# Kernel optimization log

Hardware: AMD Instinct MI355X
Metric: run time of the kernel (lower is better)

Reference implementation:

```python
import jax, jax.numpy as jnp
import numpy as np


def setup_inputs() -> dict:
    key = jax.random.key(0)
    k1, k2 = jax.random.split(key)
    B, S, D = 4, 2048, 1024
    x = jax.random.normal(k1, (B, S, D), dtype=jnp.float32)
    # uniform initializer in keras is small; scale to keep softmax well-behaved
    kernel = jax.random.normal(k2, (3, D, D), dtype=jnp.float32) * 0.02
    return {"x": x, "kernel": kernel}


def reference(x, kernel):
    # x: [B, S, D], kernel: [3, D, D]
    D = x.shape[-1]
    q = jnp.einsum('bsd,de->bse', x, kernel[0])
    k = jnp.einsum('bsd,de->bse', x, kernel[1])
    v = jnp.einsum('bsd,de->bse', x, kernel[2])
    scores = jnp.einsum('bqe,bke->bqk', q, k) / jnp.sqrt(jnp.float32(D))
    attn = jax.nn.softmax(scores, axis=-1)
    return jnp.einsum('bqk,bke->bqe', attn, v)
```

## Files before the change

### kernel.cpp

```cpp
#include <hip/hip_runtime.h>
#include <hip/hip_bf16.h>
#include <cstdint>

typedef __bf16 bf16x8 __attribute__((ext_vector_type(8)));
typedef float f32x4 __attribute__((ext_vector_type(4)));

__device__ __forceinline__ unsigned short f2bf(float f) {
  union { float f; uint32_t u; } a; a.f = f;
  uint32_t r = a.u + 0x7fffu + ((a.u >> 16) & 1u);
  return (unsigned short)(r >> 16);
}
__device__ __forceinline__ uint32_t pk2(float lo, float hi) {
  return (uint32_t)f2bf(lo) | ((uint32_t)f2bf(hi) << 16);
}
__device__ __forceinline__ void gload_lds16(const unsigned short* g, unsigned short* l) {
  __builtin_amdgcn_global_load_lds(
      (const __attribute__((address_space(1))) void*)g,
      (__attribute__((address_space(3))) void*)l, 16, 0, 0);
}

__global__ void cast_all(const float* __restrict__ x, const float* __restrict__ W,
                         unsigned short* __restrict__ xb, unsigned short* __restrict__ Wt) {
  __shared__ float tileW[64][65];
  const int bx = blockIdx.x;
  const int t = threadIdx.x;
  if (bx < 4096) {
    size_t i = ((size_t)bx * 256 + t) * 8;
    float4 a = *(const float4*)(x + i);
    float4 b = *(const float4*)(x + i + 4);
    uint4 o;
    o.x = pk2(a.x, a.y);
    o.y = pk2(a.z, a.w);
    o.z = pk2(b.x, b.y);
    o.w = pk2(b.z, b.w);
    *(uint4*)(xb + i) = o;
  } else {
    const int b = bx - 4096;
    const int z = b >> 8;
    const int rest = b & 255;
    const int bxx = rest & 15, byy = rest >> 4;
    const float* Wz = W + (size_t)z * 1048576;
    unsigned short* Wtz = Wt + (size_t)z * 1048576;
    const int x0 = bxx * 64, y0 = byy * 64;
    {
      const int r = t >> 4;
      const int c = (t & 15) * 4;
#pragma unroll
      for (int p = 0; p < 64; p += 16) {
        float4 v = *(const float4*)(Wz + (size_t)(y0 + p + r) * 1024 + x0 + c);
        tileW[p + r][c + 0] = v.x;
        tileW[p + r][c + 1] = v.y;
        tileW[p + r][c + 2] = v.z;
        tileW[p + r][c + 3] = v.w;
      }
    }
    __syncthreads();
    {
      const int dc = (t & 7) * 8;
#pragma unroll
      for (int p = 0; p < 64; p += 32) {
        const int e = p + (t >> 3);
        uint4 o;
        o.x = pk2(tileW[dc + 0][e], tileW[dc + 1][e]);
        o.y = pk2(tileW[dc + 2][e], tileW[dc + 3][e]);
        o.z = pk2(tileW[dc + 4][e], tileW[dc + 5][e]);
        o.w = pk2(tileW[dc + 6][e], tileW[dc + 7][e]);
        *(uint4*)(Wtz + (size_t)(x0 + e) * 1024 + y0 + dc) = o;
      }
    }
  }
}

__global__ void __launch_bounds__(256)
gemm_qkv(const unsigned short* __restrict__ Aall,
         const unsigned short* __restrict__ Btall,
         unsigned short* __restrict__ QK, unsigned short* __restrict__ Vt,
         int K, int ldc, long sA, long sB, long sC) {
  __shared__ unsigned short As[2][4096];
  __shared__ unsigned short Bs[2][4096];
  const int t = threadIdx.x;
  const int lane = t & 63;
  const int quad = lane >> 4;
  const int l15 = lane & 15;
  const int wave = t >> 6;
  const int wm = (wave >> 1) * 64;
  const int wn = (wave & 1) * 64;
  const int z = blockIdx.z;

  const unsigned short* A = Aall + (size_t)z * sA + (size_t)blockIdx.x * 128 * K;
  const unsigned short* Bt = Btall + (size_t)z * sB + (size_t)blockIdx.y * 128 * K;

  const int srow = t >> 2;
  const int scol = (((t & 3) ^ ((srow >> 1) & 3)) * 8);
  const unsigned short* ga = A + (size_t)srow * K + scol;
  const unsigned short* gb = Bt + (size_t)srow * K + scol;
  const size_t rowskip = (size_t)64 * K;

  const int aOff = (wm + l15) * 32 + (quad ^ ((l15 >> 1) & 3)) * 8;
  const int bOff = (wn + l15) * 32 + (quad ^ ((l15 >> 1) & 3)) * 8;

  f32x4 acc[4][4];
#pragma unroll
  for (int i = 0; i < 4; i++)
#pragma unroll
    for (int j = 0; j < 4; j++) acc[i][j] = (f32x4){0.f, 0.f, 0.f, 0.f};

  gload_lds16(ga, &As[0][t * 8]);
  gload_lds16(ga + rowskip, &As[0][2048 + t * 8]);
  gload_lds16(gb, &Bs[0][t * 8]);
  gload_lds16(gb + rowskip, &Bs[0][2048 + t * 8]);

  int buf = 0;
  for (int k0 = 0; k0 < K; k0 += 32, buf ^= 1) {
    __syncthreads();
    if (k0 + 32 < K) {
      const int kn = k0 + 32;
      gload_lds16(ga + kn, &As[buf ^ 1][t * 8]);
      gload_lds16(ga + rowskip + kn, &As[buf ^ 1][2048 + t * 8]);
      gload_lds16(gb + kn, &Bs[buf ^ 1][t * 8]);
      gload_lds16(gb + rowskip + kn, &Bs[buf ^ 1][2048 + t * 8]);
    }
    const unsigned short* aB = &As[buf][aOff];
    const unsigned short* bB = &Bs[buf][bOff];
    bf16x8 a[4], b[4];
#pragma unroll
    for (int i = 0; i < 4; i++) a[i] = *(const bf16x8*)(aB + i * 512);
#pragma unroll
    for (int j = 0; j < 4; j++) b[j] = *(const bf16x8*)(bB + j * 512);
#pragma unroll
    for (int i = 0; i < 4; i++)
#pragma unroll
      for (int j = 0; j < 4; j++)
        acc[i][j] = __builtin_amdgcn_mfma_f32_16x16x32_bf16(a[i], b[j], acc[i][j], 0, 0, 0);
  }

  const int mbase = blockIdx.x * 128 + wm + quad * 4;
  const int nbase = blockIdx.y * 128 + wn + l15;

  if (z < 2) {
    unsigned short* C = QK + (size_t)z * sC;
#pragma unroll
    for (int mi = 0; mi < 4; mi++)
#pragma unroll
      for (int ni = 0; ni < 4; ni++) {
        const int m = mbase + mi * 16, n = nbase + ni * 16;
#pragma unroll
        for (int r = 0; r < 4; r++)
          C[(size_t)(m + r) * ldc + n] = f2bf(acc[mi][ni][r]);
      }
  } else {
#pragma unroll
    for (int mi = 0; mi < 4; mi++) {
      const int m = mbase + mi * 16;
      const int b = m >> 11, s = m & 2047;
#pragma unroll
      for (int ni = 0; ni < 4; ni++) {
        const int n = nbase + ni * 16;
        uint2 val;
        val.x = pk2(acc[mi][ni][0], acc[mi][ni][1]);
        val.y = pk2(acc[mi][ni][2], acc[mi][ni][3]);
        *(uint2*)(Vt + (size_t)b * 2097152 + (size_t)n * 2048 + s) = val;
      }
    }
  }
}

#define PHASE_OPEN() do { \
    __builtin_amdgcn_sched_barrier(0); \
    __builtin_amdgcn_s_barrier(); \
    asm volatile("s_waitcnt lgkmcnt(0)" ::: "memory"); \
    __builtin_amdgcn_sched_barrier(0); \
    __builtin_amdgcn_s_setprio(1); \
  } while (0)
#define PHASE_CLOSE() do { \
    __builtin_amdgcn_s_setprio(0); \
    __builtin_amdgcn_sched_barrier(0); \
    __builtin_amdgcn_s_barrier(); \
  } while (0)

__global__ void __launch_bounds__(512, 2)
gemm8_scores(const unsigned short* __restrict__ Aall,
             const unsigned short* __restrict__ Btall,
             unsigned short* __restrict__ Call, float* __restrict__ aux,
             int K, int ldc, long sA, long sB, long sC, float scale) {
  __shared__ unsigned short As[2][2][8192];
  __shared__ unsigned short Bs[2][2][8192];
  const int t = threadIdx.x;
  const int lane = t & 63;
  const int quad = lane >> 4;
  const int l15 = lane & 15;
  const int wave = t >> 6;
  const int wm = wave >> 2;
  const int wn = wave & 3;

  const int p_ = blockIdx.x + (blockIdx.y << 3) + (blockIdx.z << 6);
  const int l_ = ((p_ & 7) << 5) | (p_ >> 3);
  const int bxi = l_ & 7, byi = (l_ >> 3) & 7;
  const int z = l_ >> 6;
  const int NT = K >> 6;

  const unsigned short* Ab = Aall + (size_t)z * sA + (size_t)bxi * 256 * K;
  const unsigned short* Bb = Btall + (size_t)z * sB + (size_t)byi * 256 * K;

  const int sc = (((t & 3) ^ ((t >> 3) & 3)) * 8);
  const unsigned short* gA = Ab + (size_t)(t >> 2) * K + sc;
  const unsigned short* gB = Bb + (size_t)(t >> 2) * K + sc;
  const size_t half2 = (size_t)128 * K;

  const int swz = (quad ^ ((l15 >> 1) & 3)) * 8;
  const int aRd = (wm * 128 + l15) * 32 + swz;
  const int bRd = (wn * 64 + l15) * 32 + swz;

  f32x4 acc[8][4];
#pragma unroll
  for (int i = 0; i < 8; ++i)
#pragma unroll
    for (int j = 0; j < 4; ++j) acc[i][j] = (f32x4){0.f, 0.f, 0.f, 0.f};

#define STG_A(TT, KH) do { \
    const unsigned short* g_ = gA + (TT) * 64 + (KH) * 32; \
    unsigned short* d_ = &As[(TT) & 1][KH][t * 8]; \
    gload_lds16(g_, d_); \
    gload_lds16(g_ + half2, d_ + 4096); \
  } while (0)
#define STG_B(TT, KH) do { \
    const unsigned short* g_ = gB + (TT) * 64 + (KH) * 32; \
    unsigned short* d_ = &Bs[(TT) & 1][KH][t * 8]; \
    gload_lds16(g_, d_); \
    gload_lds16(g_ + half2, d_ + 4096); \
  } while (0)

  STG_B(0, 0); STG_A(0, 0); STG_B(0, 1); STG_A(0, 1);
  STG_B(1, 0); STG_A(1, 0); STG_B(1, 1);
  asm volatile("s_waitcnt vmcnt(6)" ::: "memory");
  __builtin_amdgcn_s_barrier();

  for (int kt = 0; kt < NT; ++kt) {
    const int buf = kt & 1;
    bf16x8 bb[4], a[4];

#pragma unroll
    for (int j = 0; j < 4; ++j) bb[j] = *(const bf16x8*)&Bs[buf][0][bRd + j * 512];
#pragma unroll
    for (int i = 0; i < 4; ++i) a[i] = *(const bf16x8*)&As[buf][0][aRd + i * 512];
    if (kt + 1 < NT) STG_A(kt + 1, 1);
    PHASE_OPEN();
#pragma unroll
    for (int i = 0; i < 4; ++i)
#pragma unroll
      for (int j = 0; j < 4; ++j)
        acc[i][j] = __builtin_amdgcn_mfma_f32_16x16x32_bf16(a[i], bb[j], acc[i][j], 0, 0, 0);
    PHASE_CLOSE();

#pragma unroll
    for (int i = 0; i < 4; ++i) a[i] = *(const bf16x8*)&As[buf][0][aRd + 2048 + i * 512];
    if (kt + 2 < NT) STG_B(kt + 2, 0);
    PHASE_OPEN();
#pragma unroll
    for (int i = 0; i < 4; ++i)
#pragma unroll
      for (int j = 0; j < 4; ++j)
        acc[4 + i][j] = __builtin_amdgcn_mfma_f32_16x16x32_bf16(a[i], bb[j], acc[4 + i][j], 0, 0, 0);
    PHASE_CLOSE();

#pragma unroll
    for (int j = 0; j < 4; ++j) bb[j] = *(const bf16x8*)&Bs[buf][1][bRd + j * 512];
#pragma unroll
    for (int i = 0; i < 4; ++i) a[i] = *(const bf16x8*)&As[buf][1][aRd + i * 512];
    if (kt + 2 < NT) STG_A(kt + 2, 0);
    PHASE_OPEN();
#pragma unroll
    for (int i = 0; i < 4; ++i)
#pragma unroll
      for (int j = 0; j < 4; ++j)
        acc[i][j] = __builtin_amdgcn_mfma_f32_16x16x32_bf16(a[i], bb[j], acc[i][j], 0, 0, 0);
    PHASE_CLOSE();

#pragma unroll
    for (int i = 0; i < 4; ++i) a[i] = *(const bf16x8*)&As[buf][1][aRd + 2048 + i * 512];
    if (kt + 2 < NT) STG_B(kt + 2, 1);
    __builtin_amdgcn_sched_barrier(0);
    __builtin_amdgcn_s_barrier();
    asm volatile("s_waitcnt lgkmcnt(0)" ::: "memory");
    __builtin_amdgcn_sched_barrier(0);
    __builtin_amdgcn_s_setprio(1);
#pragma unroll
    for (int i = 0; i < 4; ++i)
#pragma unroll
      for (int j = 0; j < 4; ++j)
        acc[4 + i][j] = __builtin_amdgcn_mfma_f32_16x16x32_bf16(a[i], bb[j], acc[4 + i][j], 0, 0, 0);
    __builtin_amdgcn_s_setprio(0);
    __builtin_amdgcn_sched_barrier(0);
    if (kt < NT - 2) {
      asm volatile("s_waitcnt vmcnt(6)" ::: "memory");
    } else if (kt == NT - 2) {
      asm volatile("s_waitcnt vmcnt(0)" ::: "memory");
    }
    __builtin_amdgcn_s_barrier();
  }
#undef STG_A
#undef STG_B

  const int mb = bxi * 256 + wm * 128 + quad * 4;
  const int nb = byi * 256 + wn * 64 + l15;
  const int j = byi * 4 + wn;
#pragma unroll
  for (int mi = 0; mi < 8; ++mi) {
#pragma unroll
    for (int r = 0; r < 4; ++r) {
      const int m = mb + mi * 16 + r;
      float s = 0.f;
#pragma unroll
      for (int ni = 0; ni < 4; ++ni) {
        const float e = __expf(acc[mi][ni][r] * scale);
        Call[(size_t)z * sC + (size_t)m * ldc + nb + ni * 16] = f2bf(e);
        s += e;
      }
      s += __shfl_xor(s, 1);
      s += __shfl_xor(s, 2);
      s += __shfl_xor(s, 4);
      s += __shfl_xor(s, 8);
      if (l15 == 0) aux[(size_t)j * 8192 + (size_t)z * 2048 + m] = s;
    }
  }
}

__global__ void __launch_bounds__(512, 2)
gemm8_pv(const unsigned short* __restrict__ Aall,
         const unsigned short* __restrict__ Btall,
         float* __restrict__ Call, const float* __restrict__ partial) {
  const int K = 2048, NT = 32;
  __shared__ unsigned short As[2][2][4096];
  __shared__ unsigned short Bs[2][2][8192];
  __shared__ float lds_inv[128];
  const int t = threadIdx.x;
  const int lane = t & 63;
  const int quad = lane >> 4;
  const int l15 = lane & 15;
  const int wave = t >> 6;
  const int wm = wave >> 2;
  const int wn = wave & 3;

  const int p_ = blockIdx.x + (blockIdx.y << 4) + (blockIdx.z << 6);
  const int l_ = ((p_ & 7) << 5) | (p_ >> 3);
  const int byi = l_ & 3, bxi = (l_ >> 2) & 15;
  const int z = l_ >> 6;

  if (t < 128) {
    const float* pp = partial + (size_t)z * 2048 + bxi * 128 + t;
    float s = 0.f;
#pragma unroll
    for (int j = 0; j < 32; ++j) s += pp[(size_t)j * 8192];
    lds_inv[t] = 1.f / s;
  }
  asm volatile("" ::: "memory");

  const unsigned short* Ab = Aall + (size_t)z * 4194304 + (size_t)bxi * 128 * K;
  const unsigned short* Bb = Btall + (size_t)z * 2097152 + (size_t)byi * 256 * K;

  const int sc = (((t & 3) ^ ((t >> 3) & 3)) * 8);
  const unsigned short* gA = Ab + (size_t)(t >> 2) * K + sc;
  const unsigned short* gB = Bb + (size_t)(t >> 2) * K + sc;
  const size_t bhalf = (size_t)128 * K;

  const int swz = (quad ^ ((l15 >> 1) & 3)) * 8;
  const int aRd = (wm * 64 + l15) * 32 + swz;
  const int bRd = (wn * 64 + l15) * 32 + swz;

  f32x4 acc[4][4];
#pragma unroll
  for (int i = 0; i < 4; ++i)
#pragma unroll
    for (int j = 0; j < 4; ++j) acc[i][j] = (f32x4){0.f, 0.f, 0.f, 0.f};

#define STGA(TT, KH) gload_lds16(gA + (TT) * 64 + (KH) * 32, &As[(TT) & 1][KH][t * 8])
#define STGB(TT, KH) do { \
    const unsigned short* g_ = gB + (TT) * 64 + (KH) * 32; \
    unsigned short* d_ = &Bs[(TT) & 1][KH][t * 8]; \
    gload_lds16(g_, d_); \
    gload_lds16(g_ + bhalf, d_ + 4096); \
  } while (0)

  STGB(0, 0); STGA(0, 0); STGB(0, 1); STGA(0, 1);
  STGB(1, 0); STGA(1, 0);
  asm volatile("s_waitcnt vmcnt(3)" ::: "memory");
  __builtin_amdgcn_s_barrier();

  for (int kt = 0; kt < NT; ++kt) {
    const int buf = kt & 1;
    bf16x8 bb[4], a[4];

#pragma unroll
    for (int j = 0; j < 4; ++j) bb[j] = *(const bf16x8*)&Bs[buf][0][bRd + j * 512];
#pragma unroll
    for (int i = 0; i < 4; ++i) a[i] = *(const bf16x8*)&As[buf][0][aRd + i * 512];
    if (kt + 1 < NT) { STGB(kt + 1, 1); STGA(kt + 1, 1); }
    PHASE_OPEN();
#pragma unroll
    for (int i = 0; i < 4; ++i)
#pragma unroll
      for (int j = 0; j < 4; ++j)
        acc[i][j] = __builtin_amdgcn_mfma_f32_16x16x32_bf16(a[i], bb[j], acc[i][j], 0, 0, 0);
    PHASE_CLOSE();

#pragma unroll
    for (int j = 0; j < 4; ++j) bb[j] = *(const bf16x8*)&Bs[buf][1][bRd + j * 512];
#pragma unroll
    for (int i = 0; i < 4; ++i) a[i] = *(const bf16x8*)&As[buf][1][aRd + i * 512];
    if (kt + 2 < NT) { STGB(kt + 2, 0); STGA(kt + 2, 0); }
    __builtin_amdgcn_sched_barrier(0);
    __builtin_amdgcn_s_barrier();
    asm volatile("s_waitcnt lgkmcnt(0)" ::: "memory");
    __builtin_amdgcn_sched_barrier(0);
    __builtin_amdgcn_s_setprio(1);
#pragma unroll
    for (int i = 0; i < 4; ++i)
#pragma unroll
      for (int j = 0; j < 4; ++j)
        acc[i][j] = __builtin_amdgcn_mfma_f32_16x16x32_bf16(a[i], bb[j], acc[i][j], 0, 0, 0);
    __builtin_amdgcn_s_setprio(0);
    __builtin_amdgcn_sched_barrier(0);
    if (kt < NT - 2) {
      asm volatile("s_waitcnt vmcnt(3)" ::: "memory");
    } else if (kt == NT - 2) {
      asm volatile("s_waitcnt vmcnt(0)" ::: "memory");
    }
    __builtin_amdgcn_s_barrier();
  }
#undef STGA
#undef STGB

  const int rb = wm * 64 + quad * 4;
  const int mb = bxi * 128 + rb;
  const int nb = byi * 256 + wn * 64 + l15;
#pragma unroll
  for (int mi = 0; mi < 4; ++mi) {
#pragma unroll
    for (int r = 0; r < 4; ++r) {
      const int m = mb + mi * 16 + r;
      const float inv = lds_inv[rb + mi * 16 + r];
#pragma unroll
      for (int ni = 0; ni < 4; ++ni)
        Call[(size_t)z * 2097152 + (size_t)m * 1024 + nb + ni * 16] = acc[mi][ni][r] * inv;
    }
  }
}

extern "C" void kernel_launch(void* const* d_in, const int* in_sizes, int n_in,
                              void* d_out, int out_size, void* d_ws, size_t ws_size,
                              hipStream_t stream) {
  const float* x = (const float*)d_in[0];
  const float* W = (const float*)d_in[1];
  float* out = (float*)d_out;
  char* ws = (char*)d_ws;
  unsigned short* xb = (unsigned short*)(ws);
  unsigned short* Wt = (unsigned short*)(ws + (16ll << 20));
  float* partial     = (float*)(ws + (16ll << 20));
  unsigned short* Q  = (unsigned short*)(ws + (22ll << 20));
  unsigned short* Vt = (unsigned short*)(ws + (54ll << 20));
  unsigned short* Sb = (unsigned short*)(ws + (70ll << 20));

  cast_all<<<4864, 256, 0, stream>>>(x, W, xb, Wt);

  gemm_qkv<<<dim3(64, 8, 3), 256, 0, stream>>>(
      xb, Wt, Q, Vt, 1024, 1024, 0L, 1048576L, 8388608L);

  gemm8_scores<<<dim3(8, 8, 4), 512, 0, stream>>>(
      Q, Q + 8388608, Sb, partial, 1024, 2048, 2097152L, 2097152L, 4194304L, 0.03125f);

  gemm8_pv<<<dim3(16, 4, 4), 512, 0, stream>>>(Sb, Vt, out, partial);
}
```

Baseline: 235.7 us.

## Rewrite QKV projection GEMM with 8-wave 128x256 tiles and phased pipeline

Replaces the 4-wave 128x128 QKV GEMM with an 8-wave kernel computing 128x256 tiles over a 64-wide K step. It splits each step into two 32-wide halves with prefetch of later halves overlapping MFMA phases, and uses s_setprio and explicit vmcnt waits. It also remaps block IDs so blocks sharing an XCD reuse A and B tiles in cache. This targets stalls on global loads and per-step barriers. The cost is more LDS per block and fixed hardcoded dimensions.

```diff
diff --git a/kernel.cpp b/kernel.cpp
--- a/kernel.cpp
+++ b/kernel.cpp
@@ -71,100 +71,6 @@
   }
 }
 
-__global__ void __launch_bounds__(256)
-gemm_qkv(const unsigned short* __restrict__ Aall,
-         const unsigned short* __restrict__ Btall,
-         unsigned short* __restrict__ QK, unsigned short* __restrict__ Vt,
-         int K, int ldc, long sA, long sB, long sC) {
-  __shared__ unsigned short As[2][4096];
-  __shared__ unsigned short Bs[2][4096];
-  const int t = threadIdx.x;
-  const int lane = t & 63;
-  const int quad = lane >> 4;
-  const int l15 = lane & 15;
-  const int wave = t >> 6;
-  const int wm = (wave >> 1) * 64;
-  const int wn = (wave & 1) * 64;
-  const int z = blockIdx.z;
-
-  const unsigned short* A = Aall + (size_t)z * sA + (size_t)blockIdx.x * 128 * K;
-  const unsigned short* Bt = Btall + (size_t)z * sB + (size_t)blockIdx.y * 128 * K;
-
-  const int srow = t >> 2;
-  const int scol = (((t & 3) ^ ((srow >> 1) & 3)) * 8);
-  const unsigned short* ga = A + (size_t)srow * K + scol;
-  const unsigned short* gb = Bt + (size_t)srow * K + scol;
-  const size_t rowskip = (size_t)64 * K;
-
-  const int aOff = (wm + l15) * 32 + (quad ^ ((l15 >> 1) & 3)) * 8;
-  const int bOff = (wn + l15) * 32 + (quad ^ ((l15 >> 1) & 3)) * 8;
-
-  f32x4 acc[4][4];
-#pragma unroll
-  for (int i = 0; i < 4; i++)
-#pragma unroll
-    for (int j = 0; j < 4; j++) acc[i][j] = (f32x4){0.f, 0.f, 0.f, 0.f};
-
-  gload_lds16(ga, &As[0][t * 8]);
-  gload_lds16(ga + rowskip, &As[0][2048 + t * 8]);
-  gload_lds16(gb, &Bs[0][t * 8]);
-  gload_lds16(gb + rowskip, &Bs[0][2048 + t * 8]);
-
-  int buf = 0;
-  for (int k0 = 0; k0 < K; k0 += 32, buf ^= 1) {
-    __syncthreads();
-    if (k0 + 32 < K) {
-      const int kn = k0 + 32;
-      gload_lds16(ga + kn, &As[buf ^ 1][t * 8]);
-      gload_lds16(ga + rowskip + kn, &As[buf ^ 1][2048 + t * 8]);
-      gload_lds16(gb + kn, &Bs[buf ^ 1][t * 8]);
-      gload_lds16(gb + rowskip + kn, &Bs[buf ^ 1][2048 + t * 8]);
-    }
-    const unsigned short* aB = &As[buf][aOff];
-    const unsigned short* bB = &Bs[buf][bOff];
-    bf16x8 a[4], b[4];
-#pragma unroll
-    for (int i = 0; i < 4; i++) a[i] = *(const bf16x8*)(aB + i * 512);
-#pragma unroll
-    for (int j = 0; j < 4; j++) b[j] = *(const bf16x8*)(bB + j * 512);
-#pragma unroll
-    for (int i = 0; i < 4; i++)
-#pragma unroll
-      for (int j = 0; j < 4; j++)
-        acc[i][j] = __builtin_amdgcn_mfma_f32_16x16x32_bf16(a[i], b[j], acc[i][j], 0, 0, 0);
-  }
-
-  const int mbase = blockIdx.x * 128 + wm + quad * 4;
-  const int nbase = blockIdx.y * 128 + wn + l15;
-
-  if (z < 2) {
-    unsigned short* C = QK + (size_t)z * sC;
-#pragma unroll
-    for (int mi = 0; mi < 4; mi++)
-#pragma unroll
-      for (int ni = 0; ni < 4; ni++) {
-        const int m = mbase + mi * 16, n = nbase + ni * 16;
-#pragma unroll
-        for (int r = 0; r < 4; r++)
-          C[(size_t)(m + r) * ldc + n] = f2bf(acc[mi][ni][r]);
-      }
-  } else {
-#pragma unroll
-    for (int mi = 0; mi < 4; mi++) {
-      const int m = mbase + mi * 16;
-      const int b = m >> 11, s = m & 2047;
-#pragma unroll
-      for (int ni = 0; ni < 4; ni++) {
-        const int n = nbase + ni * 16;
-        uint2 val;
-        val.x = pk2(acc[mi][ni][0], acc[mi][ni][1]);
-        val.y = pk2(acc[mi][ni][2], acc[mi][ni][3]);
-        *(uint2*)(Vt + (size_t)b * 2097152 + (size_t)n * 2048 + s) = val;
-      }
-    }
-  }
-}
-
 #define PHASE_OPEN() do { \
     __builtin_amdgcn_sched_barrier(0); \
     __builtin_amdgcn_s_barrier(); \
@@ -177,6 +83,134 @@
     __builtin_amdgcn_sched_barrier(0); \
     __builtin_amdgcn_s_barrier(); \
   } while (0)
+
+__global__ void __launch_bounds__(512, 2)
+gemm8_qkv(const unsigned short* __restrict__ Aall,
+          const unsigned short* __restrict__ Btall,
+          unsigned short* __restrict__ QK, unsigned short* __restrict__ Vt) {
+  const int K = 1024, NT = 16;
+  __shared__ unsigned short As[2][2][4096];
+  __shared__ unsigned short Bs[2][2][8192];
+  const int t = threadIdx.x;
+  const int lane = t & 63;
+  const int quad = lane >> 4;
+  const int l15 = lane & 15;
+  const int wave = t >> 6;
+  const int wm = wave >> 2;
+  const int wn = wave & 3;
+
+  const int p_ = blockIdx.x + (blockIdx.y << 6) + (blockIdx.z << 8);
+  const int l_ = (p_ & 7) * 96 + (p_ >> 3);
+  const int z = l_ >> 8;
+  const int r_ = l_ & 255;
+  const int byi = r_ & 3;
+  const int bxi = ((r_ >> 2) & 7) | ((r_ >> 5) << 3);
+
+  const unsigned short* Ab = Aall + (size_t)bxi * 128 * K;
+  const unsigned short* Bb = Btall + (size_t)z * 1048576 + (size_t)byi * 256 * K;
+
+  const int sc = (((t & 3) ^ ((t >> 3) & 3)) * 8);
+  const unsigned short* gA = Ab + (size_t)(t >> 2) * K + sc;
+  const unsigned short* gB = Bb + (size_t)(t >> 2) * K + sc;
+  const size_t bhalf = (size_t)128 * K;
+
+  const int swz = (quad ^ ((l15 >> 1) & 3)) * 8;
+  const int aRd = (wm * 64 + l15) * 32 + swz;
+  const int bRd = (wn * 64 + l15) * 32 + swz;
+
+  f32x4 acc[4][4];
+#pragma unroll
+  for (int i = 0; i < 4; ++i)
+#pragma unroll
+    for (int j = 0; j < 4; ++j) acc[i][j] = (f32x4){0.f, 0.f, 0.f, 0.f};
+
+#define STGA(TT, KH) gload_lds16(gA + (TT) * 64 + (KH) * 32, &As[(TT) & 1][KH][t * 8])
+#define STGB(TT, KH) do { \
+    const unsigned short* g_ = gB + (TT) * 64 + (KH) * 32; \
+    unsigned short* d_ = &Bs[(TT) & 1][KH][t * 8]; \
+    gload_lds16(g_, d_); \
+    gload_lds16(g_ + bhalf, d_ + 4096); \
+  } while (0)
+
+  STGB(0, 0); STGA(0, 0); STGB(0, 1); STGA(0, 1);
+  STGB(1, 0); STGA(1, 0);
+  asm volatile("s_waitcnt vmcnt(3)" ::: "memory");
+  __builtin_amdgcn_s_barrier();
+
+  for (int kt = 0; kt < NT; ++kt) {
+    const int buf = kt & 1;
+    bf16x8 bb[4], a[4];
+
+#pragma unroll
+    for (int j = 0; j < 4; ++j) bb[j] = *(const bf16x8*)&Bs[buf][0][bRd + j * 512];
+#pragma unroll
+    for (int i = 0; i < 4; ++i) a[i] = *(const bf16x8*)&As[buf][0][aRd + i * 512];
+    if (kt + 1 < NT) { STGB(kt + 1, 1); STGA(kt + 1, 1); }
+    PHASE_OPEN();
+#pragma unroll
+    for (int i = 0; i < 4; ++i)
+#pragma unroll
+      for (int j = 0; j < 4; ++j)
+        acc[i][j] = __builtin_amdgcn_mfma_f32_16x16x32_bf16(a[i], bb[j], acc[i][j], 0, 0, 0);
+    PHASE_CLOSE();
+
+#pragma unroll
+    for (int j = 0; j < 4; ++j) bb[j] = *(const bf16x8*)&Bs[buf][1][bRd + j * 512];
+#pragma unroll
+    for (int i = 0; i < 4; ++i) a[i] = *(const bf16x8*)&As[buf][1][aRd + i * 512];
+    if (kt + 2 < NT) { STGB(kt + 2, 0); STGA(kt + 2, 0); }
+    __builtin_amdgcn_sched_barrier(0);
+    __builtin_amdgcn_s_barrier();
+    asm volatile("s_waitcnt lgkmcnt(0)" ::: "memory");
+    __builtin_amdgcn_sched_barrier(0);
+    __builtin_amdgcn_s_setprio(1);
+#pragma unroll
+    for (int i = 0; i < 4; ++i)
+#pragma unroll
+      for (int j = 0; j < 4; ++j)
+        acc[i][j] = __builtin_amdgcn_mfma_f32_16x16x32_bf16(a[i], bb[j], acc[i][j], 0, 0, 0);
+    __builtin_amdgcn_s_setprio(0);
+    __builtin_amdgcn_sched_barrier(0);
+    if (kt < NT - 2) {
+      asm volatile("s_waitcnt vmcnt(3)" ::: "memory");
+    } else if (kt == NT - 2) {
+      asm volatile("s_waitcnt vmcnt(0)" ::: "memory");
+    }
+    __builtin_amdgcn_s_barrier();
+  }
+#undef STGA
+#undef STGB
+
+  const int mb = bxi * 128 + wm * 64 + quad * 4;
+  const int nb = byi * 256 + wn * 64 + l15;
+
+  if (z < 2) {
+    unsigned short* C = QK + (size_t)z * 8388608;
+#pragma unroll
+    for (int mi = 0; mi < 4; ++mi)
+#pragma unroll
+      for (int ni = 0; ni < 4; ++ni) {
+        const int m = mb + mi * 16, n = nb + ni * 16;
+#pragma unroll
+        for (int r = 0; r < 4; ++r)
+          C[(size_t)(m + r) * 1024 + n] = f2bf(acc[mi][ni][r]);
+      }
+  } else {
+#pragma unroll
+    for (int mi = 0; mi < 4; ++mi) {
+      const int m = mb + mi * 16;
+      const int b = m >> 11, s = m & 2047;
+#pragma unroll
+      for (int ni = 0; ni < 4; ++ni) {
+        const int n = nb + ni * 16;
+        uint2 val;
+        val.x = pk2(acc[mi][ni][0], acc[mi][ni][1]);
+        val.y = pk2(acc[mi][ni][2], acc[mi][ni][3]);
+        *(uint2*)(Vt + (size_t)b * 2097152 + (size_t)n * 2048 + s) = val;
+      }
+    }
+  }
+}
 
 __global__ void __launch_bounds__(512, 2)
 gemm8_scores(const unsigned short* __restrict__ Aall,
@@ -462,8 +496,7 @@
 
   cast_all<<<4864, 256, 0, stream>>>(x, W, xb, Wt);
 
-  gemm_qkv<<<dim3(64, 8, 3), 256, 0, stream>>>(
-      xb, Wt, Q, Vt, 1024, 1024, 0L, 1048576L, 8388608L);
+  gemm8_qkv<<<dim3(64, 4, 3), 512, 0, stream>>>(xb, Wt, Q, Vt);
 
   gemm8_scores<<<dim3(8, 8, 4), 512, 0, stream>>>(
       Q, Q + 8388608, Sb, partial, 1024, 2048, 2097152L, 2097152L, 4194304L, 0.03125f);
```

After: 238.6 us. About the same (+1.2%).
